# Kernel optimization log

Hardware: AMD Instinct MI355X
Metric: run time of the kernel (lower is better)

Reference implementation:

```python
import jax, jax.numpy as jnp
import numpy as np

N = 50000
E = 800000
IN_DIM = 256
HID = 64
HEADS = 6
OUT_DIM = 32
NEG_SLOPE = 0.2


def gat_conv(x, src, dst, W, att_src, att_dst, bias, heads, ch, n_nodes):
    """PyG GATConv (eval mode): lin proj, per-edge LeakyReLU attention,
    segment softmax over destination neighborhoods, scatter-add aggregate.
    src/dst already include self-loops. Returns [n_nodes, heads, ch]."""
    h = (x @ W).reshape(n_nodes, heads, ch)            # [N,H,C]
    a_src = jnp.sum(h * att_src, axis=-1)              # [N,H]
    a_dst = jnp.sum(h * att_dst, axis=-1)              # [N,H]
    e = jax.nn.leaky_relu(a_src[src] + a_dst[dst], NEG_SLOPE)   # [E,H]
    m = jax.ops.segment_max(e, dst, num_segments=n_nodes)       # [N,H]
    ex = jnp.exp(e - m[dst])                                    # [E,H]
    denom = jax.ops.segment_sum(ex, dst, num_segments=n_nodes)  # [N,H]
    alpha = ex / denom[dst]                                     # [E,H]
    out = jax.ops.segment_sum(h[src] * alpha[:, :, None], dst, num_segments=n_nodes)
    return out + bias.reshape(1, heads, ch)


def setup_inputs() -> dict:
    key = jax.random.key(0)
    ks = jax.random.split(key, 10)
    x = jax.random.normal(ks[0], (N, IN_DIM), dtype=jnp.float32)
    edge_index = jax.random.randint(ks[1], (2, E), 0, N, dtype=jnp.int64)
    s1 = 1.0 / np.sqrt(IN_DIM)
    W1 = jax.random.normal(ks[2], (IN_DIM, HEADS * HID), dtype=jnp.float32) * s1
    att_src1 = jax.random.normal(ks[3], (1, HEADS, HID), dtype=jnp.float32) * 0.1
    att_dst1 = jax.random.normal(ks[4], (1, HEADS, HID), dtype=jnp.float32) * 0.1
    b1 = jnp.zeros((HEADS * HID,), dtype=jnp.float32)
    s2 = 1.0 / np.sqrt(HEADS * HID)
    W2 = jax.random.normal(ks[5], (HEADS * HID, OUT_DIM), dtype=jnp.float32) * s2
    att_src2 = jax.random.normal(ks[6], (1, 1, OUT_DIM), dtype=jnp.float32) * 0.1
    att_dst2 = jax.random.normal(ks[7], (1, 1, OUT_DIM), dtype=jnp.float32) * 0.1
    b2 = jnp.zeros((OUT_DIM,), dtype=jnp.float32)
    return {"x": x, "edge_index": edge_index, "W1": W1, "att_src1": att_src1,
            "att_dst1": att_dst1, "b1": b1, "W2": W2, "att_src2": att_src2,
            "att_dst2": att_dst2, "b2": b2}


def reference(x, edge_index, W1, att_src1, att_dst1, b1, W2, att_src2, att_dst2, b2):
    # PyG GATConv default add_self_loops=True
    loops = jnp.arange(N, dtype=edge_index.dtype)
    src = jnp.concatenate([edge_index[0], loops])
    dst = jnp.concatenate([edge_index[1], loops])
    h1 = gat_conv(x, src, dst, W1, att_src1, att_dst1, b1, HEADS, HID, N)
    h1 = jax.nn.relu(h1.reshape(N, HEADS * HID))  # concat=True, then ReLU; dropout = identity (eval)
    h2 = gat_conv(h1, src, dst, W2, att_src2, att_dst2, b2, 1, OUT_DIM, N)
    return h2.reshape(N, OUT_DIM)  # concat=False with 1 head == mean == squeeze
```

## Files before the change

kernel.cpp:

```cpp
#include <hip/hip_runtime.h>
#include <hip/hip_bf16.h>

#define NN 50000
#define EE 800000
#define IN_DIM 256
#define HID 64
#define HEADS 6
#define D1 384
#define OUT_DIM 32
#define NEG_SLOPE 0.2f
#define CAP 128
#define NBLK 196

typedef unsigned int uint32;
typedef unsigned short ushort_t;
typedef short short8 __attribute__((ext_vector_type(8)));
typedef float f32x4 __attribute__((ext_vector_type(4)));
typedef ushort_t ushort8 __attribute__((ext_vector_type(8)));

__device__ __forceinline__ ushort_t f2bf(float f) {
    uint32 u = __builtin_bit_cast(uint32, f);
    u += 0x7fffu + ((u >> 16) & 1u);
    return (ushort_t)(u >> 16);
}
__device__ __forceinline__ float bf2f(ushort_t s) {
    uint32 u = ((uint32)s) << 16;
    return __builtin_bit_cast(float, u);
}
__device__ __forceinline__ float lo16(uint32 d) { return __builtin_bit_cast(float, d << 16); }
__device__ __forceinline__ float hi16(uint32 d) { return __builtin_bit_cast(float, d & 0xffff0000u); }


__global__ void deg_init_kernel(int* __restrict__ deg) {
    int i = blockIdx.x * 256 + threadIdx.x;
    if (i < NN) deg[i] = 1;
}

__global__ void hist_kernel(const int* __restrict__ dst, int* __restrict__ deg) {
    int i = blockIdx.x * 256 + threadIdx.x;
    if (i < EE) atomicAdd(&deg[dst[i]], 1);
}

__global__ __launch_bounds__(256) void scan1_kernel(const int* __restrict__ deg,
                                                    int* __restrict__ blockSums) {
    int t = threadIdx.x;
    int i = blockIdx.x * 256 + t;
    int v = (i < NN) ? deg[i] : 0;
#pragma unroll
    for (int o = 32; o; o >>= 1) v += __shfl_xor(v, o);
    __shared__ int ws[4];
    if ((t & 63) == 0) ws[t >> 6] = v;
    __syncthreads();
    if (t == 0) blockSums[blockIdx.x] = ws[0] + ws[1] + ws[2] + ws[3];
}

__global__ __launch_bounds__(256) void scan2_kernel(const int* __restrict__ blockSums,
                                                    int* __restrict__ blockPrefix,
                                                    int* __restrict__ offsets) {
    int t = threadIdx.x;
    int lane = t & 63, w = t >> 6;
    int v = (t < NBLK) ? blockSums[t] : 0;
    int x = v;
#pragma unroll
    for (int o = 1; o < 64; o <<= 1) {
        int y = __shfl_up(x, o);
        if (lane >= o) x += y;
    }
    __shared__ int ws[4];
    if (lane == 63) ws[w] = x;
    __syncthreads();
    int wpre = 0;
#pragma unroll
    for (int k = 0; k < 4; ++k) if (k < w) wpre += ws[k];
    int incl = x + wpre;
    if (t < NBLK) blockPrefix[t] = incl - v;
    if (t == NBLK - 1) offsets[NN] = incl;
}

__global__ __launch_bounds__(256) void scan3_kernel(const int* __restrict__ deg,
                                                    const int* __restrict__ blockPrefix,
                                                    int* __restrict__ offsets,
                                                    int* __restrict__ cursor) {
    int t = threadIdx.x;
    int i = blockIdx.x * 256 + t;
    int lane = t & 63, w = t >> 6;
    int v = (i < NN) ? deg[i] : 0;
    int x = v;
#pragma unroll
    for (int o = 1; o < 64; o <<= 1) {
        int y = __shfl_up(x, o);
        if (lane >= o) x += y;
    }
    __shared__ int ws[4];
    if (lane == 63) ws[w] = x;
    __syncthreads();
    int wpre = 0;
#pragma unroll
    for (int k = 0; k < 4; ++k) if (k < w) wpre += ws[k];
    int excl = x + wpre - v + blockPrefix[blockIdx.x];
    if (i < NN) { offsets[i] = excl; cursor[i] = excl; }
}

__global__ void scatter_kernel(const int* __restrict__ src, const int* __restrict__ dst,
                               int* __restrict__ cursor, int* __restrict__ srcIdx) {
    int i = blockIdx.x * 256 + threadIdx.x;
    if (i >= EE + NN) return;
    int s, d;
    if (i < EE) { s = src[i]; d = dst[i]; }
    else        { s = i - EE; d = s; }
    int pos = atomicAdd(&cursor[d], 1);
    srcIdx[pos] = s;
}


__global__ __launch_bounds__(256) void w1t_kernel(const float* __restrict__ W1,
                                                  ushort_t* __restrict__ W1Tb) {
    __shared__ float tile[32][33];
    int tx = threadIdx.x & 31, ty = threadIdx.x >> 5;
    int n0 = blockIdx.x * 32;
    int k0 = blockIdx.y * 32;
#pragma unroll
    for (int i = 0; i < 4; ++i)
        tile[ty + i * 8][tx] = W1[(k0 + ty + i * 8) * D1 + n0 + tx];
    __syncthreads();
#pragma unroll
    for (int i = 0; i < 4; ++i)
        W1Tb[(n0 + ty + i * 8) * IN_DIM + k0 + tx] = f2bf(tile[tx][ty + i * 8]);
}

__global__ __launch_bounds__(256) void w2t_kernel(const float* __restrict__ W2,
                                                  ushort_t* __restrict__ W2Tb) {
    int idx = blockIdx.x * 256 + threadIdx.x;
    if (idx < D1 * OUT_DIM) {
        int k = idx >> 5, n = idx & 31;
        W2Tb[n * D1 + k] = f2bf(W2[idx]);
    }
}


#define G1_BM 64
#define G1_BK 64

__global__ __launch_bounds__(256) void gemm1_kernel(const float* __restrict__ A,
                                                    const ushort_t* __restrict__ Bt,
                                                    ushort_t* __restrict__ Cb) {
    __shared__ __align__(16) ushort_t As[G1_BM][G1_BK];
    __shared__ __align__(16) ushort_t Bs[D1][G1_BK];
    int t = threadIdx.x;
    int m0 = blockIdx.x * G1_BM;
    int wid = t >> 6, lane = t & 63;
    int lrow = lane & 15, lk = lane >> 4;
    f32x4 acc[4][6] = {};
    for (int k0 = 0; k0 < IN_DIM; k0 += G1_BK) {
        {
            int r = t >> 3, c = t & 7;
#pragma unroll
            for (int p = 0; p < 2; ++p) {
                int row = p * 32 + r;
                int gr = m0 + row;
                float4 v0 = make_float4(0.f, 0.f, 0.f, 0.f), v1 = v0;
                if (gr < NN) {
                    const float* g = &A[(size_t)gr * IN_DIM + k0 + c * 8];
                    v0 = *reinterpret_cast<const float4*>(g);
                    v1 = *reinterpret_cast<const float4*>(g + 4);
                }
                ushort8 u;
                u[0] = f2bf(v0.x); u[1] = f2bf(v0.y); u[2] = f2bf(v0.z); u[3] = f2bf(v0.w);
                u[4] = f2bf(v1.x); u[5] = f2bf(v1.y); u[6] = f2bf(v1.z); u[7] = f2bf(v1.w);
                *reinterpret_cast<ushort8*>(&As[row][(c ^ (row & 7)) * 8]) = u;
            }
        }
        {
            int r = t >> 3, c = t & 7;
#pragma unroll
            for (int p = 0; p < 12; ++p) {
                int row = p * 32 + r;
                ushort8 u = *reinterpret_cast<const ushort8*>(&Bt[row * IN_DIM + k0 + c * 8]);
                *reinterpret_cast<ushort8*>(&Bs[row][(c ^ (row & 7)) * 8]) = u;
            }
        }
        __syncthreads();
#pragma unroll
        for (int kk = 0; kk < G1_BK; kk += 32) {
            int ckb = (kk >> 3) + lk;
            short8 af[4];
#pragma unroll
            for (int fm = 0; fm < 4; ++fm) {
                int m = fm * 16 + lrow;
                af[fm] = *reinterpret_cast<const short8*>(&As[m][(ckb ^ (m & 7)) * 8]);
            }
#pragma unroll
            for (int fn = 0; fn < 6; ++fn) {
                int n = wid * 96 + fn * 16 + lrow;
                short8 bfv = *reinterpret_cast<const short8*>(&Bs[n][(ckb ^ (n & 7)) * 8]);
#pragma unroll
                for (int fm = 0; fm < 4; ++fm)
                    acc[fm][fn] = __builtin_amdgcn_mfma_f32_16x16x32_bf16(af[fm], bfv, acc[fm][fn], 0, 0, 0);
            }
        }
        __syncthreads();
    }
#pragma unroll
    for (int fm = 0; fm < 4; ++fm) {
#pragma unroll
        for (int r = 0; r < 4; ++r) {
            int row = m0 + fm * 16 + lk * 4 + r;
            if (row < NN) {
#pragma unroll
                for (int fn = 0; fn < 6; ++fn) {
                    int col = wid * 96 + fn * 16 + lrow;
                    Cb[(size_t)row * D1 + col] = f2bf(acc[fm][fn][r]);
                }
            }
        }
    }
}


__global__ __launch_bounds__(256) void avec1_kernel(const uint32* __restrict__ H1d,
                                                    const float* __restrict__ att_src,
                                                    const float* __restrict__ att_dst,
                                                    float* __restrict__ a_src,
                                                    float* __restrict__ a_dst) {
    int n = blockIdx.x * 4 + (threadIdx.x >> 6);
    int lane = threadIdx.x & 63;
    int hb = lane >> 5;
    const float2* asv = (const float2*)att_src;
    const float2* adv = (const float2*)att_dst;
    float ps[3], pd[3];
#pragma unroll
    for (int k = 0; k < 3; ++k) {
        uint32 d = H1d[(size_t)n * 192 + k * 64 + lane];
        float vlo = lo16(d), vhi = hi16(d);
        float2 a1 = asv[k * 64 + lane];
        float2 a2 = adv[k * 64 + lane];
        ps[k] = vlo * a1.x + vhi * a1.y;
        pd[k] = vlo * a2.x + vhi * a2.y;
    }
#pragma unroll
    for (int o = 16; o; o >>= 1) {
#pragma unroll
        for (int k = 0; k < 3; ++k) {
            ps[k] += __shfl_xor(ps[k], o);
            pd[k] += __shfl_xor(pd[k], o);
        }
    }
    if ((lane & 31) == 0) {
#pragma unroll
        for (int k = 0; k < 3; ++k) {
            a_src[n * HEADS + 2 * k + hb] = ps[k];
            a_dst[n * HEADS + 2 * k + hb] = pd[k];
        }
    }
}


__global__ __launch_bounds__(256, 4) void agg1_kernel(const uint32* __restrict__ H1d,
                                                      const float* __restrict__ a_src,
                                                      const float* __restrict__ a_dst,
                                                      const int* __restrict__ offsets,
                                                      const int* __restrict__ srcIdx,
                                                      const float* __restrict__ b1,
                                                      uint32* __restrict__ out1d) {
    __shared__ float pl[4][HEADS][CAP + 1];
    __shared__ int   sl[4][CAP];
    int w = threadIdx.x >> 6, lane = threadIdx.x & 63;
    int hb = lane >> 5;
    int n = blockIdx.x * 4 + w;
    const float2* asv = (const float2*)a_src;
    float ad[HEADS];
#pragma unroll
    for (int h = 0; h < HEADS; ++h) ad[h] = a_dst[n * HEADS + h];
    float ldn[HEADS] = {0.f, 0.f, 0.f, 0.f, 0.f, 0.f};
    float acc[6] = {0.f, 0.f, 0.f, 0.f, 0.f, 0.f};
    int beg = offsets[n], end = offsets[n + 1];
    for (int cbeg = beg; cbeg < end; cbeg += CAP) {
        int L = end - cbeg; if (L > CAP) L = CAP;
        for (int tI = lane; tI < L; tI += 64) {
            int s = srcIdx[cbeg + tI];
            sl[w][tI] = s;
            float2 e0 = asv[s * 3 + 0];
            float2 e1 = asv[s * 3 + 1];
            float2 e2 = asv[s * 3 + 2];
            float ev[6] = {e0.x, e0.y, e1.x, e1.y, e2.x, e2.y};
#pragma unroll
            for (int h = 0; h < HEADS; ++h) {
                float e = ev[h] + ad[h];
                e = e > 0.f ? e : NEG_SLOPE * e;
                float p = __expf(e);
                pl[w][h][tI] = p;
                ldn[h] += p;
            }
        }
        int j = 0;
        for (; j + 2 <= L; j += 2) {
            int s0 = sl[w][j], s1 = sl[w][j + 1];
            const uint32* h0 = H1d + (size_t)s0 * 192 + lane;
            const uint32* h1 = H1d + (size_t)s1 * 192 + lane;
            uint32 x0 = h0[0], x1 = h0[64], x2 = h0[128];
            uint32 y0 = h1[0], y1 = h1[64], y2 = h1[128];
            float p0 = pl[w][hb][j],     p1 = pl[w][2 + hb][j],     p2 = pl[w][4 + hb][j];
            float q0 = pl[w][hb][j + 1], q1 = pl[w][2 + hb][j + 1], q2 = pl[w][4 + hb][j + 1];
            acc[0] += p0 * lo16(x0); acc[1] += p0 * hi16(x0);
            acc[2] += p1 * lo16(x1); acc[3] += p1 * hi16(x1);
            acc[4] += p2 * lo16(x2); acc[5] += p2 * hi16(x2);
            acc[0] += q0 * lo16(y0); acc[1] += q0 * hi16(y0);
            acc[2] += q1 * lo16(y1); acc[3] += q1 * hi16(y1);
            acc[4] += q2 * lo16(y2); acc[5] += q2 * hi16(y2);
        }
        if (j < L) {
            int s0 = sl[w][j];
            const uint32* h0 = H1d + (size_t)s0 * 192 + lane;
            uint32 x0 = h0[0], x1 = h0[64], x2 = h0[128];
            float p0 = pl[w][hb][j], p1 = pl[w][2 + hb][j], p2 = pl[w][4 + hb][j];
            acc[0] += p0 * lo16(x0); acc[1] += p0 * hi16(x0);
            acc[2] += p1 * lo16(x1); acc[3] += p1 * hi16(x1);
            acc[4] += p2 * lo16(x2); acc[5] += p2 * hi16(x2);
        }
    }
#pragma unroll
    for (int h = 0; h < HEADS; ++h) {
#pragma unroll
        for (int o = 32; o; o >>= 1) ldn[h] += __shfl_xor(ldn[h], o);
    }
    float dsel[3];
#pragma unroll
    for (int k = 0; k < 3; ++k) dsel[k] = hb ? ldn[2 * k + 1] : ldn[2 * k];
    const float2* b1v = (const float2*)b1;
#pragma unroll
    for (int k = 0; k < 3; ++k) {
        float2 bb = b1v[k * 64 + lane];
        float v0 = fmaxf(acc[2 * k]     / dsel[k] + bb.x, 0.f);
        float v1 = fmaxf(acc[2 * k + 1] / dsel[k] + bb.y, 0.f);
        out1d[(size_t)n * 192 + k * 64 + lane] = (uint32)f2bf(v0) | ((uint32)f2bf(v1) << 16);
    }
}


#define G2_ROWS 256

__global__ __launch_bounds__(256) void gemm2_kernel(const ushort_t* __restrict__ Xb,
                                                    const ushort_t* __restrict__ W2Tb,
                                                    const float* __restrict__ att_src2,
                                                    const float* __restrict__ att_dst2,
                                                    ushort_t* __restrict__ H2b,
                                                    float* __restrict__ a_src2,
                                                    float* __restrict__ a_dst2) {
    __shared__ __align__(16) ushort_t Ws[OUT_DIM][D1];
    __shared__ __align__(16) ushort_t Xs[G2_ROWS][64];
    int t = threadIdx.x;
    int wid = t >> 6, lane = t & 63;
    int lrow = lane & 15, lk = lane >> 4;
    int m0 = blockIdx.x * G2_ROWS;
#pragma unroll
    for (int p = 0; p < 6; ++p) {
        int chunk = p * 256 + t;
        int nr = chunk / 48, c = chunk % 48;
        ushort8 u = *reinterpret_cast<const ushort8*>(&W2Tb[nr * D1 + c * 8]);
        int span = c >> 3, cc = c & 7;
        *reinterpret_cast<ushort8*>(&Ws[nr][(cc ^ (nr & 7)) * 8 + span * 64]) = u;
    }
    f32x4 acc[4][2] = {};
    for (int kc = 0; kc < 6; ++kc) {
        int k0 = kc * 64;
        {
            int r = t >> 3, c = t & 7;
#pragma unroll
            for (int p = 0; p < 8; ++p) {
                int row = p * 32 + r;
                int gr = m0 + row;
                ushort8 u = {0, 0, 0, 0, 0, 0, 0, 0};
                if (gr < NN) u = *reinterpret_cast<const ushort8*>(&Xb[(size_t)gr * D1 + k0 + c * 8]);
                *reinterpret_cast<ushort8*>(&Xs[row][(c ^ (row & 7)) * 8]) = u;
            }
        }
        __syncthreads();
#pragma unroll
        for (int kk = 0; kk < 64; kk += 32) {
            int ckb = (kk >> 3) + lk;
            short8 af[4];
#pragma unroll
            for (int fm = 0; fm < 4; ++fm) {
                int mm = wid * 64 + fm * 16 + lrow;
                af[fm] = *reinterpret_cast<const short8*>(&Xs[mm][(ckb ^ (mm & 7)) * 8]);
            }
#pragma unroll
            for (int fn = 0; fn < 2; ++fn) {
                int nn2 = fn * 16 + lrow;
                short8 bfv = *reinterpret_cast<const short8*>(&Ws[nn2][(ckb ^ (nn2 & 7)) * 8 + kc * 64]);
#pragma unroll
                for (int fm = 0; fm < 4; ++fm)
                    acc[fm][fn] = __builtin_amdgcn_mfma_f32_16x16x32_bf16(af[fm], bfv, acc[fm][fn], 0, 0, 0);
            }
        }
        __syncthreads();
    }
    float as2a = att_src2[lrow], as2b = att_src2[16 + lrow];
    float ad2a = att_dst2[lrow], ad2b = att_dst2[16 + lrow];
#pragma unroll
    for (int fm = 0; fm < 4; ++fm) {
#pragma unroll
        for (int r = 0; r < 4; ++r) {
            int row = m0 + wid * 64 + fm * 16 + lk * 4 + r;
            float h0 = acc[fm][0][r], h1 = acc[fm][1][r];
            float vs = h0 * as2a + h1 * as2b;
            float vd = h0 * ad2a + h1 * ad2b;
#pragma unroll
            for (int o = 8; o; o >>= 1) {
                vs += __shfl_xor(vs, o);
                vd += __shfl_xor(vd, o);
            }
            if (row < NN) {
                H2b[(size_t)row * OUT_DIM + lrow]      = f2bf(h0);
                H2b[(size_t)row * OUT_DIM + 16 + lrow] = f2bf(h1);
                if (lrow == 0) { a_src2[row] = vs; a_dst2[row] = vd; }
            }
        }
    }
}


__global__ __launch_bounds__(256, 4) void agg2_kernel(const ushort_t* __restrict__ H2b,
                                                      const float* __restrict__ a_src,
                                                      const float* __restrict__ a_dst,
                                                      const int* __restrict__ offsets,
                                                      const int* __restrict__ srcIdx,
                                                      const float* __restrict__ b2,
                                                      float* __restrict__ out) {
    __shared__ float pl[4][CAP];
    __shared__ int   sl[4][CAP];
    int w = threadIdx.x >> 6, lane = threadIdx.x & 63;
    int n = blockIdx.x * 4 + w;
    int q = lane & 15, par = lane >> 4;
    const uint32* H2d = (const uint32*)H2b;
    float ad = a_dst[n];
    float ldn = 0.f, ax = 0.f, ay = 0.f;
    int beg = offsets[n], end = offsets[n + 1];
    for (int cbeg = beg; cbeg < end; cbeg += CAP) {
        int L = end - cbeg; if (L > CAP) L = CAP;
        for (int tI = lane; tI < L; tI += 64) {
            int s = srcIdx[cbeg + tI];
            sl[w][tI] = s;
            float e = a_src[s] + ad;
            e = e > 0.f ? e : NEG_SLOPE * e;
            float p = __expf(e);
            pl[w][tI] = p;
            ldn += p;
        }
        for (int j = 0; j < L; j += 4) {
            int jj = j + par;
            if (jj < L) {
                int s = sl[w][jj];
                float p = pl[w][jj];
                uint32 d = H2d[(size_t)s * 16 + q];
                ax += p * lo16(d);
                ay += p * hi16(d);
            }
        }
    }
#pragma unroll
    for (int o = 32; o; o >>= 1) ldn += __shfl_xor(ldn, o);
    ax += __shfl_xor(ax, 16); ax += __shfl_xor(ax, 32);
    ay += __shfl_xor(ay, 16); ay += __shfl_xor(ay, 32);
    if (lane < 16) {
        float2 bb = ((const float2*)b2)[q];
        float2 o;
        o.x = ax / ldn + bb.x;
        o.y = ay / ldn + bb.y;
        ((float2*)out)[(size_t)n * 16 + q] = o;
    }
}


static inline size_t align256(size_t x) { return (x + 255) & ~size_t(255); }

extern "C" void kernel_launch(void* const* d_in, const int* in_sizes, int n_in,
                              void* d_out, int out_size, void* d_ws, size_t ws_size,
                              hipStream_t stream) {
    const float* x        = (const float*)d_in[0];
    const int*   ei       = (const int*)d_in[1];
    const float* W1       = (const float*)d_in[2];
    const float* att_src1 = (const float*)d_in[3];
    const float* att_dst1 = (const float*)d_in[4];
    const float* b1       = (const float*)d_in[5];
    const float* W2       = (const float*)d_in[6];
    const float* att_src2 = (const float*)d_in[7];
    const float* att_dst2 = (const float*)d_in[8];
    const float* b2       = (const float*)d_in[9];
    float* out = (float*)d_out;

    const int* e_src = ei;
    const int* e_dst = ei + EE;

    char* p = (char*)d_ws;
    ushort_t* H1b   = (ushort_t*)p; p += align256(sizeof(ushort_t) * (size_t)NN * D1);
    ushort_t* OUT1b = (ushort_t*)p; p += align256(sizeof(ushort_t) * (size_t)NN * D1);
    ushort_t* H2b   = (ushort_t*)p; p += align256(sizeof(ushort_t) * (size_t)NN * OUT_DIM);
    ushort_t* W1Tb  = (ushort_t*)p; p += align256(sizeof(ushort_t) * D1 * IN_DIM);
    ushort_t* W2Tb  = (ushort_t*)p; p += align256(sizeof(ushort_t) * D1 * OUT_DIM);
    float* AS1  = (float*)p; p += align256(sizeof(float) * NN * HEADS);
    float* AD1  = (float*)p; p += align256(sizeof(float) * NN * HEADS);
    float* AS2  = (float*)p; p += align256(sizeof(float) * NN);
    float* AD2  = (float*)p; p += align256(sizeof(float) * NN);
    int*   DEG  = (int*)p;   p += align256(sizeof(int) * NN);
    int*   OFF  = (int*)p;   p += align256(sizeof(int) * (NN + 1));
    int*   CUR  = (int*)p;   p += align256(sizeof(int) * NN);
    int*   BSUM = (int*)p;   p += align256(sizeof(int) * NBLK);
    int*   BPRE = (int*)p;   p += align256(sizeof(int) * NBLK);
    int*   SIDX = (int*)p;   p += align256(sizeof(int) * (EE + NN));

    w1t_kernel<<<dim3(D1 / 32, IN_DIM / 32), 256, 0, stream>>>(W1, W1Tb);
    w2t_kernel<<<48, 256, 0, stream>>>(W2, W2Tb);
    deg_init_kernel<<<(NN + 255) / 256, 256, 0, stream>>>(DEG);
    hist_kernel<<<(EE + 255) / 256, 256, 0, stream>>>(e_dst, DEG);
    scan1_kernel<<<NBLK, 256, 0, stream>>>(DEG, BSUM);
    scan2_kernel<<<1, 256, 0, stream>>>(BSUM, BPRE, OFF);
    scan3_kernel<<<NBLK, 256, 0, stream>>>(DEG, BPRE, OFF, CUR);
    scatter_kernel<<<(EE + NN + 255) / 256, 256, 0, stream>>>(e_src, e_dst, CUR, SIDX);

    gemm1_kernel<<<(NN + G1_BM - 1) / G1_BM, 256, 0, stream>>>(x, W1Tb, H1b);
    avec1_kernel<<<NN / 4, 256, 0, stream>>>((const uint32*)H1b, att_src1, att_dst1, AS1, AD1);
    agg1_kernel<<<NN / 4, 256, 0, stream>>>((const uint32*)H1b, AS1, AD1, OFF, SIDX, b1, (uint32*)OUT1b);

    gemm2_kernel<<<(NN + G2_ROWS - 1) / G2_ROWS, 256, 0, stream>>>(OUT1b, W2Tb, att_src2, att_dst2, H2b, AS2, AD2);
    agg2_kernel<<<NN / 4, 256, 0, stream>>>(H2b, AS2, AD2, OFF, SIDX, b2, out);
}
```

Baseline: 339.4 us.

## Fuse attention logits into GEMM1 epilogue, unroll gathers, memset degrees

Computes the per-head a_src/a_dst dot products for layer 1 inside the GEMM1 epilogue from fp32 accumulators. Partial sums are reduced with shuffles and shared memory, which removes the separate avec1 kernel and its re-read of H1. Also replaces the deg_init kernel with a memset and adds the self-loop +1 in the scan kernels. Gather loops in agg1 and agg2 are unrolled (4 and 2 edges) to keep more loads in flight. The logits now come from unrounded fp32 values rather than bf16-rounded H1, so results shift slightly, and the epilogue uses more registers.

```diff
diff --git a/kernel.cpp b/kernel.cpp
--- a/kernel.cpp
+++ b/kernel.cpp
@@ -31,11 +31,6 @@
 __device__ __forceinline__ float hi16(uint32 d) { return __builtin_bit_cast(float, d & 0xffff0000u); }
 
 
-__global__ void deg_init_kernel(int* __restrict__ deg) {
-    int i = blockIdx.x * 256 + threadIdx.x;
-    if (i < NN) deg[i] = 1;
-}
-
 __global__ void hist_kernel(const int* __restrict__ dst, int* __restrict__ deg) {
     int i = blockIdx.x * 256 + threadIdx.x;
     if (i < EE) atomicAdd(&deg[dst[i]], 1);
@@ -45,7 +40,7 @@
                                                     int* __restrict__ blockSums) {
     int t = threadIdx.x;
     int i = blockIdx.x * 256 + t;
-    int v = (i < NN) ? deg[i] : 0;
+    int v = (i < NN) ? (deg[i] + 1) : 0;
 #pragma unroll
     for (int o = 32; o; o >>= 1) v += __shfl_xor(v, o);
     __shared__ int ws[4];
@@ -84,7 +79,7 @@
     int t = threadIdx.x;
     int i = blockIdx.x * 256 + t;
     int lane = t & 63, w = t >> 6;
-    int v = (i < NN) ? deg[i] : 0;
+    int v = (i < NN) ? (deg[i] + 1) : 0;
     int x = v;
 #pragma unroll
     for (int o = 1; o < 64; o <<= 1) {
@@ -143,9 +138,15 @@
 
 __global__ __launch_bounds__(256) void gemm1_kernel(const float* __restrict__ A,
                                                     const ushort_t* __restrict__ Bt,
-                                                    ushort_t* __restrict__ Cb) {
+                                                    const float* __restrict__ att_src,
+                                                    const float* __restrict__ att_dst,
+                                                    ushort_t* __restrict__ Cb,
+                                                    float* __restrict__ a_src1,
+                                                    float* __restrict__ a_dst1) {
     __shared__ __align__(16) ushort_t As[G1_BM][G1_BK];
     __shared__ __align__(16) ushort_t Bs[D1][G1_BK];
+    __shared__ float redS[G1_BM][8];
+    __shared__ float redD[G1_BM][8];
     int t = threadIdx.x;
     int m0 = blockIdx.x * G1_BM;
     int wid = t >> 6, lane = t & 63;
@@ -200,11 +201,36 @@
         }
         __syncthreads();
     }
+    float atS[6], atD[6];
+#pragma unroll
+    for (int fn = 0; fn < 6; ++fn) {
+        int col = wid * 96 + fn * 16 + lrow;
+        atS[fn] = att_src[col];
+        atD[fn] = att_dst[col];
+    }
+    int split = (wid & 1) ? 2 : 4;
 #pragma unroll
     for (int fm = 0; fm < 4; ++fm) {
 #pragma unroll
         for (int r = 0; r < 4; ++r) {
-            int row = m0 + fm * 16 + lk * 4 + r;
+            int rowl = fm * 16 + lk * 4 + r;
+            int row = m0 + rowl;
+            float vsA = 0.f, vsB = 0.f, vdA = 0.f, vdB = 0.f;
+#pragma unroll
+            for (int fn = 0; fn < 6; ++fn) {
+                float v = acc[fm][fn][r];
+                if (fn < split) { vsA += v * atS[fn]; vdA += v * atD[fn]; }
+                else            { vsB += v * atS[fn]; vdB += v * atD[fn]; }
+            }
+#pragma unroll
+            for (int o = 8; o; o >>= 1) {
+                vsA += __shfl_xor(vsA, o); vsB += __shfl_xor(vsB, o);
+                vdA += __shfl_xor(vdA, o); vdB += __shfl_xor(vdB, o);
+            }
+            if (lrow == 0) {
+                redS[rowl][wid * 2 + 0] = vsA; redS[rowl][wid * 2 + 1] = vsB;
+                redD[rowl][wid * 2 + 0] = vdA; redD[rowl][wid * 2 + 1] = vdB;
+            }
             if (row < NN) {
 #pragma unroll
                 for (int fn = 0; fn < 6; ++fn) {
@@ -214,42 +240,18 @@
             }
         }
     }
-}
-
-
-__global__ __launch_bounds__(256) void avec1_kernel(const uint32* __restrict__ H1d,
-                                                    const float* __restrict__ att_src,
-                                                    const float* __restrict__ att_dst,
-                                                    float* __restrict__ a_src,
-                                                    float* __restrict__ a_dst) {
-    int n = blockIdx.x * 4 + (threadIdx.x >> 6);
-    int lane = threadIdx.x & 63;
-    int hb = lane >> 5;
-    const float2* asv = (const float2*)att_src;
-    const float2* adv = (const float2*)att_dst;
-    float ps[3], pd[3];
-#pragma unroll
-    for (int k = 0; k < 3; ++k) {
-        uint32 d = H1d[(size_t)n * 192 + k * 64 + lane];
-        float vlo = lo16(d), vhi = hi16(d);
-        float2 a1 = asv[k * 64 + lane];
-        float2 a2 = adv[k * 64 + lane];
-        ps[k] = vlo * a1.x + vhi * a1.y;
-        pd[k] = vlo * a2.x + vhi * a2.y;
-    }
-#pragma unroll
-    for (int o = 16; o; o >>= 1) {
-#pragma unroll
-        for (int k = 0; k < 3; ++k) {
-            ps[k] += __shfl_xor(ps[k], o);
-            pd[k] += __shfl_xor(pd[k], o);
-        }
-    }
-    if ((lane & 31) == 0) {
-#pragma unroll
-        for (int k = 0; k < 3; ++k) {
-            a_src[n * HEADS + 2 * k + hb] = ps[k];
-            a_dst[n * HEADS + 2 * k + hb] = pd[k];
+    __syncthreads();
+    if (t < G1_BM) {
+        int row = m0 + t;
+        if (row < NN) {
+            float s0 = redS[t][0], s1 = redS[t][1] + redS[t][2], s2 = redS[t][3];
+            float s3 = redS[t][4], s4 = redS[t][5] + redS[t][6], s5 = redS[t][7];
+            float d0 = redD[t][0], d1 = redD[t][1] + redD[t][2], d2 = redD[t][3];
+            float d3 = redD[t][4], d4 = redD[t][5] + redD[t][6], d5 = redD[t][7];
+            float* ps = &a_src1[(size_t)row * HEADS];
+            float* pd = &a_dst1[(size_t)row * HEADS];
+            ps[0] = s0; ps[1] = s1; ps[2] = s2; ps[3] = s3; ps[4] = s4; ps[5] = s5;
+            pd[0] = d0; pd[1] = d1; pd[2] = d2; pd[3] = d3; pd[4] = d4; pd[5] = d5;
         }
     }
 }
@@ -293,22 +295,34 @@
             }
         }
         int j = 0;
-        for (; j + 2 <= L; j += 2) {
-            int s0 = sl[w][j], s1 = sl[w][j + 1];
+        for (; j + 4 <= L; j += 4) {
+            int s0 = sl[w][j], s1 = sl[w][j + 1], s2 = sl[w][j + 2], s3 = sl[w][j + 3];
             const uint32* h0 = H1d + (size_t)s0 * 192 + lane;
             const uint32* h1 = H1d + (size_t)s1 * 192 + lane;
-            uint32 x0 = h0[0], x1 = h0[64], x2 = h0[128];
-            uint32 y0 = h1[0], y1 = h1[64], y2 = h1[128];
-            float p0 = pl[w][hb][j],     p1 = pl[w][2 + hb][j],     p2 = pl[w][4 + hb][j];
-            float q0 = pl[w][hb][j + 1], q1 = pl[w][2 + hb][j + 1], q2 = pl[w][4 + hb][j + 1];
-            acc[0] += p0 * lo16(x0); acc[1] += p0 * hi16(x0);
-            acc[2] += p1 * lo16(x1); acc[3] += p1 * hi16(x1);
-            acc[4] += p2 * lo16(x2); acc[5] += p2 * hi16(x2);
-            acc[0] += q0 * lo16(y0); acc[1] += q0 * hi16(y0);
-            acc[2] += q1 * lo16(y1); acc[3] += q1 * hi16(y1);
-            acc[4] += q2 * lo16(y2); acc[5] += q2 * hi16(y2);
-        }
-        if (j < L) {
+            const uint32* h2 = H1d + (size_t)s2 * 192 + lane;
+            const uint32* h3 = H1d + (size_t)s3 * 192 + lane;
+            uint32 a0 = h0[0], a1 = h0[64], a2 = h0[128];
+            uint32 b0 = h1[0], b1v_ = h1[64], b2 = h1[128];
+            uint32 c0 = h2[0], c1 = h2[64], c2 = h2[128];
+            uint32 d0 = h3[0], d1 = h3[64], d2 = h3[128];
+            float p00 = pl[w][hb][j],     p01 = pl[w][2 + hb][j],     p02 = pl[w][4 + hb][j];
+            float p10 = pl[w][hb][j + 1], p11 = pl[w][2 + hb][j + 1], p12 = pl[w][4 + hb][j + 1];
+            float p20 = pl[w][hb][j + 2], p21 = pl[w][2 + hb][j + 2], p22 = pl[w][4 + hb][j + 2];
+            float p30 = pl[w][hb][j + 3], p31 = pl[w][2 + hb][j + 3], p32 = pl[w][4 + hb][j + 3];
+            acc[0] += p00 * lo16(a0); acc[1] += p00 * hi16(a0);
+            acc[2] += p01 * lo16(a1); acc[3] += p01 * hi16(a1);
+            acc[4] += p02 * lo16(a2); acc[5] += p02 * hi16(a2);
+            acc[0] += p10 * lo16(b0); acc[1] += p10 * hi16(b0);
+            acc[2] += p11 * lo16(b1v_); acc[3] += p11 * hi16(b1v_);
+            acc[4] += p12 * lo16(b2); acc[5] += p12 * hi16(b2);
+            acc[0] += p20 * lo16(c0); acc[1] += p20 * hi16(c0);
+            acc[2] += p21 * lo16(c1); acc[3] += p21 * hi16(c1);
+            acc[4] += p22 * lo16(c2); acc[5] += p22 * hi16(c2);
+            acc[0] += p30 * lo16(d0); acc[1] += p30 * hi16(d0);
+            acc[2] += p31 * lo16(d1); acc[3] += p31 * hi16(d1);
+            acc[4] += p32 * lo16(d2); acc[5] += p32 * hi16(d2);
+        }
+        for (; j < L; ++j) {
             int s0 = sl[w][j];
             const uint32* h0 = H1d + (size_t)s0 * 192 + lane;
             uint32 x0 = h0[0], x1 = h0[64], x2 = h0[128];
@@ -447,7 +461,16 @@
             pl[w][tI] = p;
             ldn += p;
         }
-        for (int j = 0; j < L; j += 4) {
+        int j = 0;
+        for (; j + 8 <= L; j += 8) {
+            int s0 = sl[w][j + par], s1 = sl[w][j + 4 + par];
+            float p0 = pl[w][j + par], p1 = pl[w][j + 4 + par];
+            uint32 d0 = H2d[(size_t)s0 * 16 + q];
+            uint32 d1 = H2d[(size_t)s1 * 16 + q];
+            ax += p0 * lo16(d0) + p1 * lo16(d1);
+            ay += p0 * hi16(d0) + p1 * hi16(d1);
+        }
+        for (; j < L; j += 4) {
             int jj = j + par;
             if (jj < L) {
                 int s = sl[w][jj];
@@ -509,17 +532,16 @@
     int*   BPRE = (int*)p;   p += align256(sizeof(int) * NBLK);
     int*   SIDX = (int*)p;   p += align256(sizeof(int) * (EE + NN));
 
+    hipMemsetAsync(DEG, 0, sizeof(int) * NN, stream);
     w1t_kernel<<<dim3(D1 / 32, IN_DIM / 32), 256, 0, stream>>>(W1, W1Tb);
     w2t_kernel<<<48, 256, 0, stream>>>(W2, W2Tb);
-    deg_init_kernel<<<(NN + 255) / 256, 256, 0, stream>>>(DEG);
     hist_kernel<<<(EE + 255) / 256, 256, 0, stream>>>(e_dst, DEG);
     scan1_kernel<<<NBLK, 256, 0, stream>>>(DEG, BSUM);
     scan2_kernel<<<1, 256, 0, stream>>>(BSUM, BPRE, OFF);
     scan3_kernel<<<NBLK, 256, 0, stream>>>(DEG, BPRE, OFF, CUR);
     scatter_kernel<<<(EE + NN + 255) / 256, 256, 0, stream>>>(e_src, e_dst, CUR, SIDX);
 
-    gemm1_kernel<<<(NN + G1_BM - 1) / G1_BM, 256, 0, stream>>>(x, W1Tb, H1b);
-    avec1_kernel<<<NN / 4, 256, 0, stream>>>((const uint32*)H1b, att_src1, att_dst1, AS1, AD1);
+    gemm1_kernel<<<(NN + G1_BM - 1) / G1_BM, 256, 0, stream>>>(x, W1Tb, att_src1, att_dst1, H1b, AS1, AD1);
     agg1_kernel<<<NN / 4, 256, 0, stream>>>((const uint32*)H1b, AS1, AD1, OFF, SIDX, b1, (uint32*)OUT1b);
 
     gemm2_kernel<<<(NN + G2_ROWS - 1) / G2_ROWS, 256, 0, stream>>>(OUT1b, W2Tb, att_src2, att_dst2, H2b, AS2, AD2);
```

Measured after the change: 328.7 us. 1.03x faster.
